# Optimization experiments

Measured on AMD Instinct MI355X. Metric: run time of the kernel, lower is better.

## Reference

```python
import jax, jax.numpy as jnp
import numpy as np

MAX_DIST = 10
N_OUT = 8


def setup_inputs() -> dict:
    key = jax.random.key(0)
    k1, k2 = jax.random.split(key)
    B, N = 32, 512
    adjacency = jax.random.uniform(k1, (B, N, N), dtype=jnp.float32)
    node_mask = jnp.ones((B, N), dtype=bool)
    # learned embedding table: (max_distance + 2, n_out)
    emb = jax.random.normal(k2, (MAX_DIST + 2, N_OUT), dtype=jnp.float32)
    return {"adjacency": adjacency, "node_mask": node_mask, "emb": emb}


def reference(adjacency, node_mask, emb):
    # BFS distances computed under no_grad in the original -> stop_gradient
    adjacency = jax.lax.stop_gradient(adjacency)
    B, N, _ = adjacency.shape
    adj_bin = adjacency > 0.5
    adj_sym = adj_bin | jnp.swapaxes(adj_bin, -1, -2)
    pair_valid = node_mask[:, :, None] & node_mask[:, None, :]  # (B,N,N)
    adj_sym = adj_sym & pair_valid
    adj_f = adj_sym.astype(jnp.float32)

    UNREACH = MAX_DIST + 1
    eye = jnp.eye(N, dtype=bool)[None]                 # (1,N,N)
    dist = jnp.where(eye, 0, UNREACH).astype(jnp.int32)  # broadcasts to (B,N,N) later
    reach = jnp.broadcast_to(eye, (B, N, N))

    # iterative BFS: reach_{k+1} = (reach_k @ adj > 0) | reach_k
    for k in range(1, MAX_DIST + 1):
        reach_next = (jnp.einsum('bij,bjk->bik', reach.astype(jnp.float32), adj_f) > 0) | reach
        frontier = reach_next & ~reach
        dist = jnp.where(frontier, jnp.int32(k), dist)
        reach = reach_next

    dist = jnp.where(pair_valid, dist, UNREACH)  # invalid pairs -> UNREACHABLE
    return emb[dist]  # (B,N,N,n_out)
```

## Files before the change

kernel.cpp:

```cpp
#include <hip/hip_runtime.h>
#include <stdint.h>

#define NB 32
#define N 512
#define MAXD 10
#define NW 8

__global__ __launch_bounds__(256) void k1_pack(const float* __restrict__ adj,
                                               const int* __restrict__ mask,
                                               unsigned long long* __restrict__ gsym) {
    __shared__ float ldsA[64 * 65];
    __shared__ float ldsB[64 * 65];
    __shared__ unsigned char mI[64], mJ[64];
    int p = blockIdx.x;
    int b = blockIdx.y;
    int ti = 0;
    while (p >= 8 - ti) { p -= 8 - ti; ++ti; }
    int tj = ti + p;
    int i0 = ti * 64, j0 = tj * 64;
    int t = threadIdx.x;
    if (t < 64) mI[t] = (mask[b * N + i0 + t] != 0);
    else if (t < 128) mJ[t - 64] = (mask[b * N + j0 + (t - 64)] != 0);
    const float* Ab = adj + (size_t)b * N * N;
    #pragma unroll
    for (int s = 0; s < 4; ++s) {
        int idx = t + 256 * s;
        int r = idx >> 4, c4 = idx & 15;
        float4 va = *(const float4*)&Ab[(size_t)(i0 + r) * N + j0 + c4 * 4];
        float4 vb = *(const float4*)&Ab[(size_t)(j0 + r) * N + i0 + c4 * 4];
        int o = r * 65 + c4 * 4;
        ldsA[o] = va.x; ldsA[o + 1] = va.y; ldsA[o + 2] = va.z; ldsA[o + 3] = va.w;
        ldsB[o] = vb.x; ldsB[o + 1] = vb.y; ldsB[o + 2] = vb.z; ldsB[o + 3] = vb.w;
    }
    __syncthreads();
    int wave = t >> 6, lane = t & 63;
    for (int s = 0; s < 16; ++s) {
        int r = wave * 16 + s;
        bool bit = ((ldsA[r * 65 + lane] > 0.5f) || (ldsB[lane * 65 + r] > 0.5f))
                   && mI[r] && mJ[lane];
        unsigned long long word = __ballot(bit);
        if (lane == 0) gsym[((size_t)b * N + i0 + r) * NW + tj] = word;
    }
    for (int s = 0; s < 16; ++s) {
        int r = wave * 16 + s;
        bool bit = ((ldsB[r * 65 + lane] > 0.5f) || (ldsA[lane * 65 + r] > 0.5f))
                   && mJ[r] && mI[lane];
        unsigned long long word = __ballot(bit);
        if (lane == 0) gsym[((size_t)b * N + j0 + r) * NW + ti] = word;
    }
}

__global__ __launch_bounds__(64) void k2_bfs(const unsigned long long* __restrict__ gsym,
                                             const int* __restrict__ mask,
                                             unsigned char* __restrict__ distg) {
    __shared__ unsigned long long adjT[NW * N];
    __shared__ unsigned char distB[64 * N];
    int blk = blockIdx.x;
    int b = blk >> 3;
    int r0 = (blk & 7) * 64;
    int t = threadIdx.x;
    const unsigned long long* gs = gsym + (size_t)b * N * NW;
    for (int q = t; q < N * NW; q += 64) {
        unsigned long long w = gs[q];
        adjT[(q & 7) * N + (q >> 3)] = w;
    }
    unsigned long long* d64 = (unsigned long long*)distB;
    for (int q = t; q < 64 * N / 8; q += 64)
        d64[q] = 0x0B0B0B0B0B0B0B0BULL;
    __syncthreads();

    int i = r0 + t;
    bool mi = mask[b * N + i] != 0;
    if (mi) {
        distB[t * N + i] = 0;
        unsigned long long reach[NW] = {};
        unsigned long long frontier[NW] = {};
        reach[i >> 6] = 1ULL << (i & 63);
        frontier[i >> 6] = reach[i >> 6];
        for (int k = 1; k <= MAXD; ++k) {
            unsigned long long acc[NW] = {};
            bool sat = false;
            for (int w = 0; w < NW && !sat; ++w) {
                unsigned long long f = frontier[w];
                while (f) {
                    int j = (w << 6) + __builtin_ctzll(f);
                    f &= f - 1;
                    #pragma unroll
                    for (int e = 0; e < NW; ++e) acc[e] |= adjT[e * N + j];
                    unsigned long long all = acc[0];
                    #pragma unroll
                    for (int e = 1; e < NW; ++e) all &= acc[e];
                    if (all == ~0ULL) { sat = true; break; }
                }
            }
            bool any = false;
            #pragma unroll
            for (int w = 0; w < NW; ++w) {
                unsigned long long nf = acc[w] & ~reach[w];
                frontier[w] = nf;
                reach[w] |= nf;
                if (nf) any = true;
                while (nf) {
                    int j = (w << 6) + __builtin_ctzll(nf);
                    nf &= nf - 1;
                    distB[t * N + j] = (unsigned char)k;
                }
            }
            if (!any) break;
        }
    }
    __syncthreads();
    unsigned long long* dg = (unsigned long long*)distg + (size_t)blk * 64 * (N / 8);
    for (int q = t; q < 64 * (N / 8); q += 64)
        dg[q] = d64[q];
}

__global__ __launch_bounds__(256) void k3_expand(const unsigned char* __restrict__ distg,
                                                 const float* __restrict__ emb,
                                                 float4* __restrict__ out4) {
    __shared__ unsigned char drow[N];
    __shared__ float4 e4[(MAXD + 2) * 2];
    int row = blockIdx.x;
    int t = threadIdx.x;
    if (t < N / 4)
        ((uint32_t*)drow)[t] = ((const uint32_t*)distg)[(size_t)row * (N / 4) + t];
    if (t >= 128 && t < 128 + (MAXD + 2) * 2)
        e4[t - 128] = ((const float4*)emb)[t - 128];
    __syncthreads();
    size_t base = (size_t)row * (N * 2);
    #pragma unroll
    for (int s = 0; s < 4; ++s) {
        int q = t + 256 * s;
        int j = q >> 1, h = q & 1;
        int d = drow[j];
        out4[base + q] = e4[d * 2 + h];
    }
}

extern "C" void kernel_launch(void* const* d_in, const int* in_sizes, int n_in,
                              void* d_out, int out_size, void* d_ws, size_t ws_size,
                              hipStream_t stream) {
    const float* adj = (const float*)d_in[0];
    const int* mask = (const int*)d_in[1];
    const float* emb = (const float*)d_in[2];
    unsigned long long* gsym = (unsigned long long*)d_ws;
    unsigned char* distg = (unsigned char*)d_ws + (size_t)NB * N * NW * 8;
    k1_pack<<<dim3(36, NB), 256, 0, stream>>>(adj, mask, gsym);
    k2_bfs<<<dim3(NB * 8), 64, 0, stream>>>(gsym, mask, distg);
    k3_expand<<<dim3(NB * N), 256, 0, stream>>>(distg, emb, (float4*)d_out);
}
```

Measured before the change: 393.3 us.

## Track BFS distances with bit-sliced counters and use nontemporal output stores

```diff
diff --git a/kernel.cpp b/kernel.cpp
--- a/kernel.cpp
+++ b/kernel.cpp
@@ -1,5 +1,8 @@
 #include <hip/hip_runtime.h>
 #include <stdint.h>
+
+typedef unsigned long long u64;
+typedef float vf4 __attribute__((ext_vector_type(4)));
 
 #define NB 32
 #define N 512
@@ -8,7 +11,7 @@
 
 __global__ __launch_bounds__(256) void k1_pack(const float* __restrict__ adj,
                                                const int* __restrict__ mask,
-                                               unsigned long long* __restrict__ gsym) {
+                                               u64* __restrict__ gsym) {
     __shared__ float ldsA[64 * 65];
     __shared__ float ldsB[64 * 65];
     __shared__ unsigned char mI[64], mJ[64];
@@ -38,94 +41,126 @@
         int r = wave * 16 + s;
         bool bit = ((ldsA[r * 65 + lane] > 0.5f) || (ldsB[lane * 65 + r] > 0.5f))
                    && mI[r] && mJ[lane];
-        unsigned long long word = __ballot(bit);
+        u64 word = __ballot(bit);
         if (lane == 0) gsym[((size_t)b * N + i0 + r) * NW + tj] = word;
     }
     for (int s = 0; s < 16; ++s) {
         int r = wave * 16 + s;
         bool bit = ((ldsB[r * 65 + lane] > 0.5f) || (ldsA[lane * 65 + r] > 0.5f))
                    && mJ[r] && mI[lane];
-        unsigned long long word = __ballot(bit);
+        u64 word = __ballot(bit);
         if (lane == 0) gsym[((size_t)b * N + j0 + r) * NW + ti] = word;
     }
 }
 
-__global__ __launch_bounds__(64) void k2_bfs(const unsigned long long* __restrict__ gsym,
+__device__ __forceinline__ u64 spread8(unsigned b) {
+    u64 x = (u64)(b * 0x01010101u);
+    x |= x << 32;
+    x &= 0x8040201008040201ULL;
+    x += 0x7f7f7f7f7f7f7f7fULL;
+    return (x >> 7) & 0x0101010101010101ULL;
+}
+
+__global__ __launch_bounds__(64) void k2_bfs(const u64* __restrict__ gsym,
                                              const int* __restrict__ mask,
-                                             unsigned char* __restrict__ distg) {
-    __shared__ unsigned long long adjT[NW * N];
-    __shared__ unsigned char distB[64 * N];
+                                             u64* __restrict__ distg64) {
+    __shared__ u64 adjT[NW * N];
+    __shared__ u64 outB[64 * 65];
     int blk = blockIdx.x;
     int b = blk >> 3;
     int r0 = (blk & 7) * 64;
     int t = threadIdx.x;
-    const unsigned long long* gs = gsym + (size_t)b * N * NW;
+    const u64* gs = gsym + (size_t)b * N * NW;
     for (int q = t; q < N * NW; q += 64) {
-        unsigned long long w = gs[q];
+        u64 w = gs[q];
         adjT[(q & 7) * N + (q >> 3)] = w;
     }
-    unsigned long long* d64 = (unsigned long long*)distB;
-    for (int q = t; q < 64 * N / 8; q += 64)
-        d64[q] = 0x0B0B0B0B0B0B0B0BULL;
     __syncthreads();
 
     int i = r0 + t;
     bool mi = mask[b * N + i] != 0;
+    u64 c0[NW], c1[NW], c2[NW], c3[NW];
+    #pragma unroll
+    for (int w = 0; w < NW; ++w) { c0[w] = 0; c1[w] = 0; c2[w] = 0; c3[w] = 0; }
+
     if (mi) {
-        distB[t * N + i] = 0;
-        unsigned long long reach[NW] = {};
-        unsigned long long frontier[NW] = {};
+        u64 reach[NW] = {};
+        u64 frontier[NW] = {};
         reach[i >> 6] = 1ULL << (i & 63);
-        frontier[i >> 6] = reach[i >> 6];
-        for (int k = 1; k <= MAXD; ++k) {
-            unsigned long long acc[NW] = {};
-            bool sat = false;
-            for (int w = 0; w < NW && !sat; ++w) {
-                unsigned long long f = frontier[w];
-                while (f) {
-                    int j = (w << 6) + __builtin_ctzll(f);
-                    f &= f - 1;
-                    #pragma unroll
-                    for (int e = 0; e < NW; ++e) acc[e] |= adjT[e * N + j];
-                    unsigned long long all = acc[0];
-                    #pragma unroll
-                    for (int e = 1; e < NW; ++e) all &= acc[e];
-                    if (all == ~0ULL) { sat = true; break; }
-                }
-            }
-            bool any = false;
+        #pragma unroll
+        for (int w = 0; w < NW; ++w) frontier[w] = reach[w];
+        bool active = true;
+        for (int k = 0; k <= MAXD; ++k) {
             #pragma unroll
             for (int w = 0; w < NW; ++w) {
-                unsigned long long nf = acc[w] & ~reach[w];
-                frontier[w] = nf;
-                reach[w] |= nf;
-                if (nf) any = true;
-                while (nf) {
-                    int j = (w << 6) + __builtin_ctzll(nf);
-                    nf &= nf - 1;
-                    distB[t * N + j] = (unsigned char)k;
+                u64 u = ~reach[w];
+                u64 t0 = c0[w] & u; c0[w] ^= u;
+                u64 t1 = c1[w] & t0; c1[w] ^= t0;
+                u64 t2 = c2[w] & t1; c2[w] ^= t1;
+                c3[w] ^= t2;
+            }
+            if (k == MAXD) break;
+            if (active) {
+                u64 acc[NW] = {};
+                bool sat = false;
+                for (int w = 0; w < NW && !sat; ++w) {
+                    u64 f = frontier[w];
+                    while (f) {
+                        int j = (w << 6) + __builtin_ctzll(f);
+                        f &= f - 1;
+                        #pragma unroll
+                        for (int e = 0; e < NW; ++e) acc[e] |= adjT[e * N + j];
+                        u64 all = acc[0];
+                        #pragma unroll
+                        for (int e = 1; e < NW; ++e) all &= acc[e];
+                        if (all == ~0ULL) { sat = true; break; }
+                    }
                 }
+                bool any = false;
+                #pragma unroll
+                for (int w = 0; w < NW; ++w) {
+                    u64 nf = acc[w] & ~reach[w];
+                    frontier[w] = nf;
+                    reach[w] |= nf;
+                    any = any || (nf != 0);
+                }
+                active = any;
             }
-            if (!any) break;
+        }
+    } else {
+        #pragma unroll
+        for (int w = 0; w < NW; ++w) { c0[w] = ~0ULL; c1[w] = ~0ULL; c3[w] = ~0ULL; }
+    }
+
+    #pragma unroll
+    for (int w = 0; w < NW; ++w) {
+        #pragma unroll
+        for (int h = 0; h < 8; ++h) {
+            unsigned b0 = (unsigned)(c0[w] >> (8 * h)) & 0xFF;
+            unsigned b1 = (unsigned)(c1[w] >> (8 * h)) & 0xFF;
+            unsigned b2 = (unsigned)(c2[w] >> (8 * h)) & 0xFF;
+            unsigned b3 = (unsigned)(c3[w] >> (8 * h)) & 0xFF;
+            u64 bytes = spread8(b0) | (spread8(b1) << 1) | (spread8(b2) << 2) | (spread8(b3) << 3);
+            outB[t * 65 + w * 8 + h] = bytes;
         }
     }
     __syncthreads();
-    unsigned long long* dg = (unsigned long long*)distg + (size_t)blk * 64 * (N / 8);
-    for (int q = t; q < 64 * (N / 8); q += 64)
-        dg[q] = d64[q];
+    u64* dg = distg64 + (size_t)blk * 64 * 64;
+    for (int q = t; q < 64 * 64; q += 64)
+        dg[q] = outB[(q >> 6) * 65 + (q & 63)];
 }
 
 __global__ __launch_bounds__(256) void k3_expand(const unsigned char* __restrict__ distg,
                                                  const float* __restrict__ emb,
-                                                 float4* __restrict__ out4) {
+                                                 vf4* __restrict__ out4) {
     __shared__ unsigned char drow[N];
-    __shared__ float4 e4[(MAXD + 2) * 2];
+    __shared__ vf4 e4[(MAXD + 2) * 2];
     int row = blockIdx.x;
     int t = threadIdx.x;
     if (t < N / 4)
         ((uint32_t*)drow)[t] = ((const uint32_t*)distg)[(size_t)row * (N / 4) + t];
     if (t >= 128 && t < 128 + (MAXD + 2) * 2)
-        e4[t - 128] = ((const float4*)emb)[t - 128];
+        e4[t - 128] = ((const vf4*)emb)[t - 128];
     __syncthreads();
     size_t base = (size_t)row * (N * 2);
     #pragma unroll
@@ -133,7 +168,7 @@
         int q = t + 256 * s;
         int j = q >> 1, h = q & 1;
         int d = drow[j];
-        out4[base + q] = e4[d * 2 + h];
+        __builtin_nontemporal_store(e4[d * 2 + h], &out4[base + q]);
     }
 }
 
@@ -143,9 +178,9 @@
     const float* adj = (const float*)d_in[0];
     const int* mask = (const int*)d_in[1];
     const float* emb = (const float*)d_in[2];
-    unsigned long long* gsym = (unsigned long long*)d_ws;
+    u64* gsym = (u64*)d_ws;
     unsigned char* distg = (unsigned char*)d_ws + (size_t)NB * N * NW * 8;
     k1_pack<<<dim3(36, NB), 256, 0, stream>>>(adj, mask, gsym);
-    k2_bfs<<<dim3(NB * 8), 64, 0, stream>>>(gsym, mask, distg);
-    k3_expand<<<dim3(NB * N), 256, 0, stream>>>(distg, emb, (float4*)d_out);
+    k2_bfs<<<dim3(NB * 8), 64, 0, stream>>>(gsym, mask, (u64*)distg);
+    k3_expand<<<dim3(NB * N), 256, 0, stream>>>(distg, emb, (vf4*)d_out);
 }
```

After: 363.8 us. 7.5% less time.
